# Kernel optimization log

Measured on AMD Instinct MI355X. Metric: run time of the kernel, lower is better.

Reference implementation:

```python
import jax, jax.numpy as jnp
import numpy as np

N_NODES = 50000
N_EDGES = 800000
IN_FEATS = 64
HIDDEN = 64
NUM_CLASSES = 64


def setup_inputs() -> dict:
    key = jax.random.key(0)
    ks = jax.random.split(key, 9)
    inputs = jax.random.normal(ks[0], (N_NODES, IN_FEATS), dtype=jnp.float32)
    W1 = jax.random.normal(ks[1], (HIDDEN, IN_FEATS), dtype=jnp.float32) * 0.05
    b1 = jax.random.normal(ks[2], (HIDDEN,), dtype=jnp.float32) * 0.05
    W2 = jax.random.normal(ks[3], (NUM_CLASSES, HIDDEN), dtype=jnp.float32) * 0.05
    b2 = jax.random.normal(ks[4], (NUM_CLASSES,), dtype=jnp.float32) * 0.05
    W3 = jax.random.normal(ks[5], (1, N_NODES), dtype=jnp.float32) * 0.01
    b3 = jax.random.normal(ks[6], (1,), dtype=jnp.float32) * 0.05
    src = jax.random.randint(ks[7], (N_EDGES,), 0, N_NODES, dtype=jnp.int32)
    dst = jax.random.randint(ks[8], (N_EDGES,), 0, N_NODES, dtype=jnp.int32)
    return {"inputs": inputs, "W1": W1, "b1": b1, "W2": W2, "b2": b2,
            "W3": W3, "b3": b3, "src": src, "dst": dst}


def _aggregate(h, src, dst):
    # DGL update_all with sum reduce: dst node gets sum of src features over in-edges
    msgs = h[src]  # [E, d] gather
    return jax.ops.segment_sum(msgs, dst, num_segments=N_NODES)


def reference(inputs, W1, b1, W2, b2, W3, b3, src, dst):
    # GNN layer 1: aggregate then linear
    h = _aggregate(inputs, src, dst) @ W1.T + b1  # [N, hidden]
    h = jax.nn.relu(h)
    # GNN layer 2
    h = _aggregate(h, src, dst) @ W2.T + b2       # [N, num_classes]
    # transpose -> [num_classes, N], linear over node dim -> [num_classes, 1]
    h = h.T @ W3.T + b3
    return jax.nn.sigmoid(h)
```

## Files before the change

kernel.cpp:

```cpp
#include <hip/hip_runtime.h>


#define FEATS 64
#define NW4   12500
#define NHALF 25000
#define JD    128
#define JU    32
#define S_SLOT (64*16)
#define NB_BASES 49
#define NHIST (JD + 2*JU)

__device__ __forceinline__ unsigned f2bf(float x) {
    unsigned u = __float_as_uint(x);
    return (u + 0x7fffu + ((u >> 16) & 1u)) >> 16;
}
__device__ __forceinline__ float bf2f_lo(unsigned u) { return __uint_as_float(u << 16); }
__device__ __forceinline__ float bf2f_hi(unsigned u) { return __uint_as_float(u & 0xffff0000u); }

__global__ __launch_bounds__(512) void hist_kernel(
    const int* __restrict__ src, const int* __restrict__ dst,
    const float* __restrict__ W3, unsigned* __restrict__ cb8,
    float* __restrict__ uJ, float* __restrict__ partialPad,
    const float* __restrict__ X, ushort* __restrict__ featB, int nFeat,
    int nEdges, int chD, int chU)
{
    __shared__ unsigned smem[NHALF];
    int t = threadIdx.x;
    if (blockIdx.x >= NHIST) {
        int i = ((blockIdx.x - NHIST) * 512 + t) * 8;
        if (i + 7 < nFeat) {
            float4 a = *reinterpret_cast<const float4*>(&X[i]);
            float4 b = *reinterpret_cast<const float4*>(&X[i + 4]);
            uint4 o;
            o.x = f2bf(a.x) | (f2bf(a.y) << 16);
            o.y = f2bf(a.z) | (f2bf(a.w) << 16);
            o.z = f2bf(b.x) | (f2bf(b.y) << 16);
            o.w = f2bf(b.z) | (f2bf(b.w) << 16);
            *reinterpret_cast<uint4*>(&featB[i]) = o;
        }
        return;
    }
    if (blockIdx.x == 0) {
        for (int l = t; l < S_SLOT + 32; l += 512) partialPad[l] = 0.0f;
    }
    if (blockIdx.x < JD) {
        unsigned* cnt = smem;
        for (int l = t; l < NW4; l += 512) cnt[l] = 0u;
        __syncthreads();
        int j = blockIdx.x;
        int beg = j * chD, end = min(beg + chD, nEdges);
        for (int e = beg + t; e < end; e += 512) {
            int d = dst[e];
            atomicAdd(&cnt[d >> 2], 1u << ((d & 3) * 8));
        }
        __syncthreads();
        unsigned* out = cb8 + (size_t)j * NW4;
        for (int l = t; l < NW4; l += 512) out[l] = cnt[l];
    } else {
        float* ua = (float*)smem;
        for (int l = t; l < NHALF; l += 512) ua[l] = 0.0f;
        __syncthreads();
        int b = blockIdx.x - JD;
        int p = b & 1, j = b >> 1;
        int beg = j * chU, end = min(beg + chU, nEdges);
        for (int e = beg + t; e < end; e += 512) {
            int s = src[e];
            if ((s & 1) == p) atomicAdd(&ua[s >> 1], W3[dst[e]]);
        }
        __syncthreads();
        float* out = uJ + (size_t)b * NHALF;
        for (int l = t; l < NHALF; l += 512) out[l] = ua[l];
    }
}

__global__ __launch_bounds__(256) void bases_kernel(
    unsigned* __restrict__ cb8, const float* __restrict__ uJ,
    const float* __restrict__ W3, int* __restrict__ deg,
    float* __restrict__ u, float* __restrict__ partialPad)
{
    int w = blockIdx.x * 256 + threadIdx.x;
    float sv = 0.0f;
    if (w < NW4) {
        unsigned run = 0u;
        #pragma unroll 16
        for (int j = 0; j < JD; ++j) {
            unsigned c = cb8[(size_t)j * NW4 + w];
            cb8[(size_t)j * NW4 + w] = run;
            run += c;
        }
        int4 dg;
        dg.x = run & 0xff; dg.y = (run >> 8) & 0xff;
        dg.z = (run >> 16) & 0xff; dg.w = run >> 24;
        *reinterpret_cast<int4*>(&deg[w * 4]) = dg;

        float us0 = 0.f, us1 = 0.f, us2 = 0.f, us3 = 0.f;
        #pragma unroll 8
        for (int j = 0; j < JU; ++j) {
            const float* a0 = uJ + (size_t)(2 * j)     * NHALF;
            const float* a1 = uJ + (size_t)(2 * j + 1) * NHALF;
            float2 e0 = *reinterpret_cast<const float2*>(&a0[2 * w]);
            float2 e1 = *reinterpret_cast<const float2*>(&a1[2 * w]);
            us0 += e0.x; us2 += e0.y;
            us1 += e1.x; us3 += e1.y;
        }
        *reinterpret_cast<float4*>(&u[w * 4]) = make_float4(us0, us1, us2, us3);

        float4 w4 = *reinterpret_cast<const float4*>(&W3[w * 4]);
        sv = (w4.x + w4.y) + (w4.z + w4.w);
    }
    for (int o = 32; o > 0; o >>= 1) sv += __shfl_down(sv, o, 64);
    __shared__ float ws[4];
    if ((threadIdx.x & 63) == 0) ws[threadIdx.x >> 6] = sv;
    __syncthreads();
    if (threadIdx.x == 0)
        atomicAdd(&partialPad[S_SLOT], ws[0] + ws[1] + ws[2] + ws[3]);
}

__global__ __launch_bounds__(512) void edge_scatter_kernel(
    const int* __restrict__ src, const int* __restrict__ dst,
    const unsigned* __restrict__ cb8, ushort* __restrict__ srcSorted,
    int nEdges, int chunk)
{
    __shared__ unsigned cnt[NW4];
    int t = threadIdx.x, j = blockIdx.x;
    const unsigned* bb = cb8 + (size_t)j * NW4;
    for (int l = t; l < NW4; l += 512) cnt[l] = bb[l];
    __syncthreads();
    int beg = j * chunk, end = min(beg + chunk, nEdges);
    for (int e = beg + t * 2; e < end; e += 1024) {
        if (e + 1 < end) {
            int2 d2 = *reinterpret_cast<const int2*>(&dst[e]);
            int2 s2 = *reinterpret_cast<const int2*>(&src[e]);
            int sh0 = (d2.x & 3) * 8;
            unsigned o0 = atomicAdd(&cnt[d2.x >> 2], 1u << sh0);
            srcSorted[(d2.x << 6) + ((o0 >> sh0) & 0xff)] = (ushort)s2.x;
            int sh1 = (d2.y & 3) * 8;
            unsigned o1 = atomicAdd(&cnt[d2.y >> 2], 1u << sh1);
            srcSorted[(d2.y << 6) + ((o1 >> sh1) & 0xff)] = (ushort)s2.y;
        } else {
            int d = dst[e], s = src[e];
            int sh = (d & 3) * 8;
            unsigned old = atomicAdd(&cnt[d >> 2], 1u << sh);
            srcSorted[(d << 6) + ((old >> sh) & 0xff)] = (ushort)s;
        }
    }
}

__global__ __launch_bounds__(256) void fused_gather_linear_kernel(
    const ushort* __restrict__ featB, const ushort* __restrict__ srcSorted,
    const int* __restrict__ deg, const float* __restrict__ W1,
    const float* __restrict__ b1, const float* __restrict__ u,
    float* __restrict__ partialPad, int nNodes)
{
    __shared__ ushort idxbuf[4][8][64];
    __shared__ float rowbuf[4][8][FEATS];
    __shared__ float red[4][FEATS];
    int t = threadIdx.x, lane = t & 63, w = t >> 6;
    int g = lane >> 3;
    int l8 = lane & 7;

    float4 w1r[16];
    #pragma unroll
    for (int k4 = 0; k4 < 16; ++k4)
        w1r[k4] = *reinterpret_cast<const float4*>(&W1[lane * FEATS + k4 * 4]);
    float bias = b1[lane];

    int nOcts = (nNodes + 7) >> 3;
    int oct = blockIdx.x * 4 + w;
    float vacc = 0.0f;

    if (oct < nOcts) {
        int n_g = oct * 8 + g;
        int d = 0;
        float un = 0.0f;
        if (n_g < nNodes) {
            d = deg[n_g];
            un = u[n_g];
            if (l8 * 8 < d) {
                uint4 ip = *reinterpret_cast<const uint4*>(&srcSorted[((size_t)n_g << 6) + l8 * 8]);
                *reinterpret_cast<uint4*>(&idxbuf[w][g][l8 * 8]) = ip;
            }
        }
        __builtin_amdgcn_wave_barrier();

        int dm = d;
        dm = max(dm, __shfl_xor(dm, 8, 64));
        dm = max(dm, __shfl_xor(dm, 16, 64));
        dm = max(dm, __shfl_xor(dm, 32, 64));

        float a0=0.f,a1=0.f,a2=0.f,a3=0.f,a4=0.f,a5=0.f,a6=0.f,a7=0.f;
        uint4 r0,r1,r2,r3, s0,s1,s2,s3;
        uint4 z = make_uint4(0u,0u,0u,0u);

        #define LOADB(J, q0, q1, q2, q3)                                              \
        {   int jj = (J);                                                             \
            uint2 ids = *reinterpret_cast<const uint2*>(&idxbuf[w][g][jj]);           \
            int i0 = ids.x & 0xffff, i1 = ids.x >> 16;                                \
            int i2 = ids.y & 0xffff, i3 = ids.y >> 16;                                \
            q0 = (jj + 0 < d) ? *reinterpret_cast<const uint4*>(&featB[((size_t)i0 << 6) + l8 * 8]) : z; \
            q1 = (jj + 1 < d) ? *reinterpret_cast<const uint4*>(&featB[((size_t)i1 << 6) + l8 * 8]) : z; \
            q2 = (jj + 2 < d) ? *reinterpret_cast<const uint4*>(&featB[((size_t)i2 << 6) + l8 * 8]) : z; \
            q3 = (jj + 3 < d) ? *reinterpret_cast<const uint4*>(&featB[((size_t)i3 << 6) + l8 * 8]) : z; \
        }
        #define ACCB(q0, q1, q2, q3)                                                  \
        {   a0 += (bf2f_lo(q0.x) + bf2f_lo(q1.x)) + (bf2f_lo(q2.x) + bf2f_lo(q3.x));  \
            a1 += (bf2f_hi(q0.x) + bf2f_hi(q1.x)) + (bf2f_hi(q2.x) + bf2f_hi(q3.x));  \
            a2 += (bf2f_lo(q0.y) + bf2f_lo(q1.y)) + (bf2f_lo(q2.y) + bf2f_lo(q3.y));  \
            a3 += (bf2f_hi(q0.y) + bf2f_hi(q1.y)) + (bf2f_hi(q2.y) + bf2f_hi(q3.y));  \
            a4 += (bf2f_lo(q0.z) + bf2f_lo(q1.z)) + (bf2f_lo(q2.z) + bf2f_lo(q3.z));  \
            a5 += (bf2f_hi(q0.z) + bf2f_hi(q1.z)) + (bf2f_hi(q2.z) + bf2f_hi(q3.z));  \
            a6 += (bf2f_lo(q0.w) + bf2f_lo(q1.w)) + (bf2f_lo(q2.w) + bf2f_lo(q3.w));  \
            a7 += (bf2f_hi(q0.w) + bf2f_hi(q1.w)) + (bf2f_hi(q2.w) + bf2f_hi(q3.w));  \
        }

        LOADB(0, r0, r1, r2, r3);
        LOADB(4, s0, s1, s2, s3);
        for (int j = 0; j < dm; j += 8) {
            ACCB(r0, r1, r2, r3);
            LOADB(j + 8, r0, r1, r2, r3);
            ACCB(s0, s1, s2, s3);
            LOADB(j + 12, s0, s1, s2, s3);
        }
        #undef LOADB
        #undef ACCB

        *reinterpret_cast<float4*>(&rowbuf[w][g][l8 * 8])     = make_float4(a0,a1,a2,a3);
        *reinterpret_cast<float4*>(&rowbuf[w][g][l8 * 8 + 4]) = make_float4(a4,a5,a6,a7);
        __builtin_amdgcn_wave_barrier();

        #pragma unroll
        for (int gp = 0; gp < 8; ++gp) {
            float ug = __shfl(un, gp * 8, 64);
            float out = bias;
            #pragma unroll
            for (int k4 = 0; k4 < 16; ++k4) {
                float4 r = *reinterpret_cast<const float4*>(&rowbuf[w][gp][k4 * 4]);
                out += r.x * w1r[k4].x + r.y * w1r[k4].y
                     + r.z * w1r[k4].z + r.w * w1r[k4].w;
            }
            vacc += ug * fmaxf(out, 0.0f);
        }
    }

    red[w][lane] = vacc;
    __syncthreads();
    if (w == 0) {
        float vv = red[0][lane] + red[1][lane] + red[2][lane] + red[3][lane];
        atomicAdd(&partialPad[lane * 16], vv);
    }
}

__global__ __launch_bounds__(64) void finalize_kernel(
    const float* __restrict__ partialPad, const float* __restrict__ W2,
    const float* __restrict__ b2, const float* __restrict__ b3,
    float* __restrict__ out)
{
    __shared__ float v[FEATS];
    int c = threadIdx.x;
    v[c] = partialPad[c * 16];
    float s = partialPad[S_SLOT];
    __syncthreads();
    float acc = b3[0] + b2[c] * s;
    #pragma unroll
    for (int k = 0; k < FEATS; ++k)
        acc += W2[c * FEATS + k] * v[k];
    out[c] = 1.0f / (1.0f + expf(-acc));
}

extern "C" void kernel_launch(void* const* d_in, const int* in_sizes, int n_in,
                              void* d_out, int out_size, void* d_ws, size_t ws_size,
                              hipStream_t stream) {
    const float* inputs = (const float*)d_in[0];
    const float* W1     = (const float*)d_in[1];
    const float* b1     = (const float*)d_in[2];
    const float* W2     = (const float*)d_in[3];
    const float* b2     = (const float*)d_in[4];
    const float* W3     = (const float*)d_in[5];
    const float* b3     = (const float*)d_in[6];
    const int*   src    = (const int*)d_in[7];
    const int*   dst    = (const int*)d_in[8];

    int nNodes = in_sizes[0] / FEATS;
    int nEdges = in_sizes[7];

    unsigned* cb8       = (unsigned*)d_ws;
    float*    uJ        = (float*)(cb8 + (size_t)JD * NW4);
    int*      deg       = (int*)(uJ + (size_t)2 * JU * NHALF);
    float*    u         = (float*)(deg + 4 * NW4);
    float*    partialPad= u + 4 * NW4;
    ushort*   featB     = (ushort*)(partialPad + S_SLOT + 32);
    ushort*   srcSorted = featB + (size_t)4 * NW4 * FEATS;
    float*    outF      = (float*)d_out;

    int nFeat = nNodes * FEATS;
    int chD = (nEdges + JD - 1) / JD;
    int chU = ((nEdges + JU - 1) / JU + 1) & ~1;

    int convBlocks = (nFeat / 8 + 511) / 512;
    hist_kernel<<<NHIST + convBlocks, 512, 0, stream>>>(
        src, dst, W3, cb8, uJ, partialPad, inputs, featB, nFeat, nEdges, chD, chU);
    bases_kernel<<<NB_BASES, 256, 0, stream>>>(cb8, uJ, W3, deg, u, partialPad);
    edge_scatter_kernel<<<JD, 512, 0, stream>>>(src, dst, cb8, srcSorted, nEdges, chD);
    int nOcts = (nNodes + 7) >> 3;
    fused_gather_linear_kernel<<<(nOcts + 3) / 4, 256, 0, stream>>>(
        featB, srcSorted, deg, W1, b1, u, partialPad, nNodes);
    finalize_kernel<<<1, 64, 0, stream>>>(partialPad, W2, b2, b3, outF);
}
```

Baseline: 132.8 us.

## Merge histogram, prefix-scan and edge-scatter kernels into one cooperative kernel

Replaces the three preprocessing kernels (histogram/bf16 conversion, base prefix scan, edge scatter) with a single cooperative kernel of 256 blocks that separates the phases with grid-wide syncs. The aim is to remove two kernel launches and their inter-kernel gaps. Feature conversion now uses a grid-stride loop over fewer blocks. In exchange, grid.sync adds barrier overhead and the fixed 256-block grid limits parallelism in the scan and conversion phases. The per-block shared reduction is also replaced by per-wavefront atomics.

Measured after the change: 218.3 us. 64.4% more time.

```diff
diff --git a/kernel.cpp b/kernel.cpp
--- a/kernel.cpp
+++ b/kernel.cpp
@@ -1,4 +1,7 @@
 #include <hip/hip_runtime.h>
+#include <hip/hip_cooperative_groups.h>
+
+namespace cg = cooperative_groups;
 
 
 #define FEATS 64
@@ -7,8 +10,8 @@
 #define JD    128
 #define JU    32
 #define S_SLOT (64*16)
-#define NB_BASES 49
 #define NHIST (JD + 2*JU)
+#define NPREP 256
 
 __device__ __forceinline__ unsigned f2bf(float x) {
     unsigned u = __float_as_uint(x);
@@ -17,131 +20,123 @@
 __device__ __forceinline__ float bf2f_lo(unsigned u) { return __uint_as_float(u << 16); }
 __device__ __forceinline__ float bf2f_hi(unsigned u) { return __uint_as_float(u & 0xffff0000u); }
 
-__global__ __launch_bounds__(512) void hist_kernel(
+__global__ __launch_bounds__(512) void prep_kernel(
     const int* __restrict__ src, const int* __restrict__ dst,
     const float* __restrict__ W3, unsigned* __restrict__ cb8,
     float* __restrict__ uJ, float* __restrict__ partialPad,
-    const float* __restrict__ X, ushort* __restrict__ featB, int nFeat,
-    int nEdges, int chD, int chU)
+    const float* __restrict__ X, ushort* __restrict__ featB,
+    int* __restrict__ deg, float* __restrict__ u,
+    ushort* __restrict__ srcSorted,
+    int nFeat, int nEdges, int chD, int chU)
 {
     __shared__ unsigned smem[NHALF];
-    int t = threadIdx.x;
-    if (blockIdx.x >= NHIST) {
-        int i = ((blockIdx.x - NHIST) * 512 + t) * 8;
-        if (i + 7 < nFeat) {
-            float4 a = *reinterpret_cast<const float4*>(&X[i]);
-            float4 b = *reinterpret_cast<const float4*>(&X[i + 4]);
-            uint4 o;
-            o.x = f2bf(a.x) | (f2bf(a.y) << 16);
-            o.y = f2bf(a.z) | (f2bf(a.w) << 16);
-            o.z = f2bf(b.x) | (f2bf(b.y) << 16);
-            o.w = f2bf(b.z) | (f2bf(b.w) << 16);
-            *reinterpret_cast<uint4*>(&featB[i]) = o;
-        }
-        return;
-    }
-    if (blockIdx.x == 0) {
+    cg::grid_group grid = cg::this_grid();
+    int t = threadIdx.x, b = blockIdx.x;
+
+    if (b == 0) {
         for (int l = t; l < S_SLOT + 32; l += 512) partialPad[l] = 0.0f;
     }
-    if (blockIdx.x < JD) {
+    if (b < JD) {
         unsigned* cnt = smem;
         for (int l = t; l < NW4; l += 512) cnt[l] = 0u;
         __syncthreads();
-        int j = blockIdx.x;
-        int beg = j * chD, end = min(beg + chD, nEdges);
+        int beg = b * chD, end = min(beg + chD, nEdges);
         for (int e = beg + t; e < end; e += 512) {
             int d = dst[e];
             atomicAdd(&cnt[d >> 2], 1u << ((d & 3) * 8));
         }
         __syncthreads();
-        unsigned* out = cb8 + (size_t)j * NW4;
+        unsigned* out = cb8 + (size_t)b * NW4;
         for (int l = t; l < NW4; l += 512) out[l] = cnt[l];
-    } else {
+    } else if (b < NHIST) {
         float* ua = (float*)smem;
         for (int l = t; l < NHALF; l += 512) ua[l] = 0.0f;
         __syncthreads();
-        int b = blockIdx.x - JD;
-        int p = b & 1, j = b >> 1;
+        int bb = b - JD;
+        int p = bb & 1, j = bb >> 1;
         int beg = j * chU, end = min(beg + chU, nEdges);
         for (int e = beg + t; e < end; e += 512) {
             int s = src[e];
             if ((s & 1) == p) atomicAdd(&ua[s >> 1], W3[dst[e]]);
         }
         __syncthreads();
-        float* out = uJ + (size_t)b * NHALF;
+        float* out = uJ + (size_t)bb * NHALF;
         for (int l = t; l < NHALF; l += 512) out[l] = ua[l];
-    }
-}
-
-__global__ __launch_bounds__(256) void bases_kernel(
-    unsigned* __restrict__ cb8, const float* __restrict__ uJ,
-    const float* __restrict__ W3, int* __restrict__ deg,
-    float* __restrict__ u, float* __restrict__ partialPad)
-{
-    int w = blockIdx.x * 256 + threadIdx.x;
-    float sv = 0.0f;
-    if (w < NW4) {
-        unsigned run = 0u;
-        #pragma unroll 16
-        for (int j = 0; j < JD; ++j) {
-            unsigned c = cb8[(size_t)j * NW4 + w];
-            cb8[(size_t)j * NW4 + w] = run;
-            run += c;
-        }
-        int4 dg;
-        dg.x = run & 0xff; dg.y = (run >> 8) & 0xff;
-        dg.z = (run >> 16) & 0xff; dg.w = run >> 24;
-        *reinterpret_cast<int4*>(&deg[w * 4]) = dg;
-
-        float us0 = 0.f, us1 = 0.f, us2 = 0.f, us3 = 0.f;
-        #pragma unroll 8
-        for (int j = 0; j < JU; ++j) {
-            const float* a0 = uJ + (size_t)(2 * j)     * NHALF;
-            const float* a1 = uJ + (size_t)(2 * j + 1) * NHALF;
-            float2 e0 = *reinterpret_cast<const float2*>(&a0[2 * w]);
-            float2 e1 = *reinterpret_cast<const float2*>(&a1[2 * w]);
-            us0 += e0.x; us2 += e0.y;
-            us1 += e1.x; us3 += e1.y;
-        }
-        *reinterpret_cast<float4*>(&u[w * 4]) = make_float4(us0, us1, us2, us3);
-
-        float4 w4 = *reinterpret_cast<const float4*>(&W3[w * 4]);
-        sv = (w4.x + w4.y) + (w4.z + w4.w);
-    }
-    for (int o = 32; o > 0; o >>= 1) sv += __shfl_down(sv, o, 64);
-    __shared__ float ws[4];
-    if ((threadIdx.x & 63) == 0) ws[threadIdx.x >> 6] = sv;
-    __syncthreads();
-    if (threadIdx.x == 0)
-        atomicAdd(&partialPad[S_SLOT], ws[0] + ws[1] + ws[2] + ws[3]);
-}
-
-__global__ __launch_bounds__(512) void edge_scatter_kernel(
-    const int* __restrict__ src, const int* __restrict__ dst,
-    const unsigned* __restrict__ cb8, ushort* __restrict__ srcSorted,
-    int nEdges, int chunk)
-{
-    __shared__ unsigned cnt[NW4];
-    int t = threadIdx.x, j = blockIdx.x;
-    const unsigned* bb = cb8 + (size_t)j * NW4;
-    for (int l = t; l < NW4; l += 512) cnt[l] = bb[l];
-    __syncthreads();
-    int beg = j * chunk, end = min(beg + chunk, nEdges);
-    for (int e = beg + t * 2; e < end; e += 1024) {
-        if (e + 1 < end) {
-            int2 d2 = *reinterpret_cast<const int2*>(&dst[e]);
-            int2 s2 = *reinterpret_cast<const int2*>(&src[e]);
-            int sh0 = (d2.x & 3) * 8;
-            unsigned o0 = atomicAdd(&cnt[d2.x >> 2], 1u << sh0);
-            srcSorted[(d2.x << 6) + ((o0 >> sh0) & 0xff)] = (ushort)s2.x;
-            int sh1 = (d2.y & 3) * 8;
-            unsigned o1 = atomicAdd(&cnt[d2.y >> 2], 1u << sh1);
-            srcSorted[(d2.y << 6) + ((o1 >> sh1) & 0xff)] = (ushort)s2.y;
-        } else {
-            int d = dst[e], s = src[e];
-            int sh = (d & 3) * 8;
-            unsigned old = atomicAdd(&cnt[d >> 2], 1u << sh);
-            srcSorted[(d << 6) + ((old >> sh) & 0xff)] = (ushort)s;
+    } else {
+        int nUnits = nFeat / 8;
+        for (int i = (b - NHIST) * 512 + t; i < nUnits; i += (NPREP - NHIST) * 512) {
+            int idx = i * 8;
+            float4 a = *reinterpret_cast<const float4*>(&X[idx]);
+            float4 bb4 = *reinterpret_cast<const float4*>(&X[idx + 4]);
+            uint4 o;
+            o.x = f2bf(a.x) | (f2bf(a.y) << 16);
+            o.y = f2bf(a.z) | (f2bf(a.w) << 16);
+            o.z = f2bf(bb4.x) | (f2bf(bb4.y) << 16);
+            o.w = f2bf(bb4.z) | (f2bf(bb4.w) << 16);
+            *reinterpret_cast<uint4*>(&featB[idx]) = o;
+        }
+    }
+    grid.sync();
+
+    {
+        int w = b * 512 + t;
+        float sv = 0.0f;
+        if (w < NW4) {
+            unsigned run = 0u;
+            #pragma unroll 16
+            for (int j = 0; j < JD; ++j) {
+                unsigned c = cb8[(size_t)j * NW4 + w];
+                cb8[(size_t)j * NW4 + w] = run;
+                run += c;
+            }
+            int4 dg;
+            dg.x = run & 0xff; dg.y = (run >> 8) & 0xff;
+            dg.z = (run >> 16) & 0xff; dg.w = run >> 24;
+            *reinterpret_cast<int4*>(&deg[w * 4]) = dg;
+
+            float us0 = 0.f, us1 = 0.f, us2 = 0.f, us3 = 0.f;
+            #pragma unroll 8
+            for (int j = 0; j < JU; ++j) {
+                const float* a0 = uJ + (size_t)(2 * j)     * NHALF;
+                const float* a1 = uJ + (size_t)(2 * j + 1) * NHALF;
+                float2 e0 = *reinterpret_cast<const float2*>(&a0[2 * w]);
+                float2 e1 = *reinterpret_cast<const float2*>(&a1[2 * w]);
+                us0 += e0.x; us2 += e0.y;
+                us1 += e1.x; us3 += e1.y;
+            }
+            *reinterpret_cast<float4*>(&u[w * 4]) = make_float4(us0, us1, us2, us3);
+
+            float4 w4 = *reinterpret_cast<const float4*>(&W3[w * 4]);
+            sv = (w4.x + w4.y) + (w4.z + w4.w);
+        }
+        for (int o = 32; o > 0; o >>= 1) sv += __shfl_down(sv, o, 64);
+        if ((t & 63) == 0 && sv != 0.0f)
+            atomicAdd(&partialPad[S_SLOT], sv);
+    }
+    grid.sync();
+
+    if (b < JD) {
+        unsigned* cnt = smem;
+        const unsigned* bb = cb8 + (size_t)b * NW4;
+        for (int l = t; l < NW4; l += 512) cnt[l] = bb[l];
+        __syncthreads();
+        int beg = b * chD, end = min(beg + chD, nEdges);
+        for (int e = beg + t * 2; e < end; e += 1024) {
+            if (e + 1 < end) {
+                int2 d2 = *reinterpret_cast<const int2*>(&dst[e]);
+                int2 s2 = *reinterpret_cast<const int2*>(&src[e]);
+                int sh0 = (d2.x & 3) * 8;
+                unsigned o0 = atomicAdd(&cnt[d2.x >> 2], 1u << sh0);
+                srcSorted[(d2.x << 6) + ((o0 >> sh0) & 0xff)] = (ushort)s2.x;
+                int sh1 = (d2.y & 3) * 8;
+                unsigned o1 = atomicAdd(&cnt[d2.y >> 2], 1u << sh1);
+                srcSorted[(d2.y << 6) + ((o1 >> sh1) & 0xff)] = (ushort)s2.y;
+            } else {
+                int d = dst[e], s = src[e];
+                int sh = (d & 3) * 8;
+                unsigned old = atomicAdd(&cnt[d >> 2], 1u << sh);
+                srcSorted[(d << 6) + ((old >> sh) & 0xff)] = (ushort)s;
+            }
         }
     }
 }
@@ -296,11 +291,15 @@
     int chD = (nEdges + JD - 1) / JD;
     int chU = ((nEdges + JU - 1) / JU + 1) & ~1;
 
-    int convBlocks = (nFeat / 8 + 511) / 512;
-    hist_kernel<<<NHIST + convBlocks, 512, 0, stream>>>(
-        src, dst, W3, cb8, uJ, partialPad, inputs, featB, nFeat, nEdges, chD, chU);
-    bases_kernel<<<NB_BASES, 256, 0, stream>>>(cb8, uJ, W3, deg, u, partialPad);
-    edge_scatter_kernel<<<JD, 512, 0, stream>>>(src, dst, cb8, srcSorted, nEdges, chD);
+    void* args[] = {
+        (void*)&src, (void*)&dst, (void*)&W3, (void*)&cb8, (void*)&uJ,
+        (void*)&partialPad, (void*)&inputs, (void*)&featB, (void*)&deg,
+        (void*)&u, (void*)&srcSorted, (void*)&nFeat, (void*)&nEdges,
+        (void*)&chD, (void*)&chU
+    };
+    hipLaunchCooperativeKernel((const void*)prep_kernel, dim3(NPREP), dim3(512),
+                               args, 0, stream);
+
     int nOcts = (nNodes + 7) >> 3;
     fused_gather_linear_kernel<<<(nOcts + 3) / 4, 256, 0, stream>>>(
         featB, srcSorted, deg, W1, b1, u, partialPad, nNodes);
```
